# Optimization experiments

Measured on AMD Instinct MI355X. Metric: run time of the kernel, lower is better.

The kernel has to match this reference:

```python
import jax, jax.numpy as jnp
import numpy as np

C = 512
B, H, W = 4, 64, 64
GROUPS = 32
EPS = 1e-6
SCALE = 1.0 / np.sqrt(C)


def setup_inputs() -> dict:
    key = jax.random.key(0)
    ks = jax.random.split(key, 3)
    x = jax.random.normal(ks[0], (B, C, H, W), dtype=jnp.float32)
    # conv weights: kaiming-ish small init for numerical sanity
    qkv_w = jax.random.normal(ks[1], (3 * C, C), dtype=jnp.float32) * (1.0 / np.sqrt(C))
    proj_w = jax.random.normal(ks[2], (C, C), dtype=jnp.float32) * (1.0 / np.sqrt(C))
    return {
        "x": x,
        "norm_w": jnp.ones((C,), jnp.float32),
        "norm_b": jnp.zeros((C,), jnp.float32),
        "qkv_w": qkv_w,
        "qkv_b": jnp.zeros((3 * C,), jnp.float32),
        "proj_w": proj_w,
        "proj_b": jnp.zeros((C,), jnp.float32),
    }


def reference(x, norm_w, norm_b, qkv_w, qkv_b, proj_w, proj_b):
    b, c, h, w = x.shape
    hw = h * w
    # GroupNorm(32, eps=1e-6, affine)
    xg = x.reshape(b, GROUPS, -1)                       # [B, G, (C/G)*H*W]
    mean = jnp.mean(xg, axis=-1, keepdims=True)
    var = jnp.var(xg, axis=-1, keepdims=True)
    xn = ((xg - mean) * jax.lax.rsqrt(var + EPS)).reshape(b, c, h, w)
    xn = xn * norm_w[:, None, None] + norm_b[:, None, None]
    # 1x1 conv qkv == channel matmul
    qkv = jnp.einsum('oc,bchw->bohw', qkv_w, xn) + qkv_b[:, None, None]
    q, k, v = jnp.split(qkv, 3, axis=1)                 # each [B, C, H, W]
    q = q.reshape(b, c, hw)                              # [B, C, HW]
    k = k.reshape(b, c, hw)
    v = v.reshape(b, c, hw)
    # attn[b, i, j] = softmax_j( q_i . k_j * scale )
    scores = jnp.einsum('bci,bcj->bij', q, k) * SCALE    # [B, HW, HW]
    attn = jax.nn.softmax(scores, axis=-1)
    # h[b, c, i] = sum_j v[b, c, j] * attn[b, i, j]
    hmap = jnp.einsum('bcj,bij->bci', v, attn).reshape(b, c, h, w)
    out = x + jnp.einsum('oc,bchw->bohw', proj_w, hmap) + proj_b[:, None, None]
    return out
```

## Files before the change

kernel.cpp:

```cpp
#include <hip/hip_runtime.h>
#include <hip/hip_fp8.h>
#include <cstdint>
#include <cmath>

#define B_   4
#define C_   512
#define HW_  4096
#define G_   32
#define CPG_ 16
#define EPS_ 1e-6f
#define SCALE_ 0.04419417382415922f
#define PSCALE_ 0.0625f
#define SEXPC_ 0.063758715306f


typedef __bf16 bf16_t;
typedef __bf16 bf16x8 __attribute__((ext_vector_type(8)));
typedef float  f32x4  __attribute__((ext_vector_type(4)));
typedef int    i32x4  __attribute__((ext_vector_type(4)));
typedef int    i32x8  __attribute__((ext_vector_type(8)));
typedef unsigned int u32;
typedef __hip_fp8_e4m3 fp8_t;

__device__ __forceinline__ void cp16(const void* g, void* l) {
  __builtin_amdgcn_global_load_lds((__attribute__((address_space(1))) u32*)(g),
                                   (__attribute__((address_space(3))) u32*)(l),
                                   16, 0, 0);
}

__device__ __forceinline__ float fexp2(float x) {
  float r;
  asm("v_exp_f32 %0, %1\n\ts_nop 1" : "=v"(r) : "v"(x));
  return r;
}

__device__ __forceinline__ void zero_acc(f32x4 acc[4][4]) {
  f32x4 z = {0.f, 0.f, 0.f, 0.f};
#pragma unroll
  for (int i = 0; i < 4; ++i)
#pragma unroll
    for (int j = 0; j < 4; ++j) acc[i][j] = z;
}

template <bool ROWSUM, int SA = 0x7F, int SB = 0x7F>
__device__ __forceinline__ void gemm_bt_mx(const unsigned char* __restrict__ A,
                                           const unsigned char* __restrict__ B,
                                           int K, int lda, int ldb,
                                           f32x4 acc[4][4], f32x4 accl[4],
                                           unsigned char* AsB, unsigned char* BsB) {
  const int tid  = threadIdx.x;
  const int wave = tid >> 6;
  const int lane = tid & 63;
  const int wm = (wave >> 1) * 64;
  const int wn = (wave & 1) * 64;
  const int srow = lane >> 3;
  const int gch  = ((lane & 7) - srow) & 7;
  const unsigned char* gA = A + (size_t)(wave * 32 + srow) * lda + gch * 16;
  const unsigned char* gB = B + (size_t)(wave * 32 + srow) * ldb + gch * 16;
  const int lofs = wave * 32 * 128;
  const int fr = lane & 15;
  const int q  = lane >> 4;
  const int co0 = ((2 * q     + fr) & 7) * 16;
  const int co1 = ((2 * q + 1 + fr) & 7) * 16;
  const i32x8 vones = {0x38383838, 0x38383838, 0x38383838, 0x38383838,
                       0x38383838, 0x38383838, 0x38383838, 0x38383838};

  const int nT = K >> 7;
#pragma unroll
  for (int cc = 0; cc < 4; ++cc) {
    cp16(gA + (size_t)(cc * 8) * lda, AsB + lofs + cc * 1024);
    cp16(gB + (size_t)(cc * 8) * ldb, BsB + lofs + cc * 1024);
  }
  gA += 128; gB += 128;

#pragma unroll 1
  for (int t = 0; t < nT; ++t) {
    const int cur = t & 1;
    if (t + 1 < nT) {
#pragma unroll
      for (int cc = 0; cc < 4; ++cc) {
        cp16(gA + (size_t)(cc * 8) * lda, AsB + (cur ^ 1) * 16384 + lofs + cc * 1024);
        cp16(gB + (size_t)(cc * 8) * ldb, BsB + (cur ^ 1) * 16384 + lofs + cc * 1024);
      }
      gA += 128; gB += 128;
      asm volatile("s_waitcnt vmcnt(8)" ::: "memory");
    } else {
      asm volatile("s_waitcnt vmcnt(0)" ::: "memory");
    }
    __builtin_amdgcn_s_barrier();

    i32x8 a[4], b[4];
    const unsigned char* Ab = AsB + cur * 16384;
    const unsigned char* Bb = BsB + cur * 16384;
#pragma unroll
    for (int i = 0; i < 4; ++i) {
      const int ro = (wm + i * 16 + fr) * 128;
      i32x4 lo = *(const i32x4*)(Ab + ro + co0);
      i32x4 hi = *(const i32x4*)(Ab + ro + co1);
      a[i] = __builtin_shufflevector(lo, hi, 0, 1, 2, 3, 4, 5, 6, 7);
    }
#pragma unroll
    for (int j = 0; j < 4; ++j) {
      const int ro = (wn + j * 16 + fr) * 128;
      i32x4 lo = *(const i32x4*)(Bb + ro + co0);
      i32x4 hi = *(const i32x4*)(Bb + ro + co1);
      b[j] = __builtin_shufflevector(lo, hi, 0, 1, 2, 3, 4, 5, 6, 7);
    }
    __builtin_amdgcn_s_setprio(1);
#pragma unroll
    for (int i = 0; i < 4; ++i) {
#pragma unroll
      for (int j = 0; j < 4; ++j)
        acc[i][j] = __builtin_amdgcn_mfma_scale_f32_16x16x128_f8f6f4(
            a[i], b[j], acc[i][j], 0, 0, 0, SA, 0, SB);
      if (ROWSUM)
        accl[i] = __builtin_amdgcn_mfma_scale_f32_16x16x128_f8f6f4(
            a[i], vones, accl[i], 0, 0, 0, SA, 0, 0x7F);
    }
    __builtin_amdgcn_s_setprio(0);
    __builtin_amdgcn_s_barrier();
  }
}


__global__ void __launch_bounds__(256) prep_kernel(const float* __restrict__ x,
                                                   float* __restrict__ stats,
                                                   const float* __restrict__ qkv_w,
                                                   const float* __restrict__ proj_w,
                                                   fp8_t* __restrict__ wqkv8,
                                                   fp8_t* __restrict__ wproj8) {
  __shared__ float rs[256], rss[256];
  const int n = blockIdx.x;
  if (n < 1024) {
    const int bg = n >> 3;
    const int ch = n & 7;
    const float4* base = (const float4*)(x + (size_t)bg * (CPG_ * HW_)) +
                         (size_t)ch * (CPG_ * HW_ / 4 / 8);
    float s = 0.f, ss = 0.f;
    for (int i = threadIdx.x; i < CPG_ * HW_ / 4 / 8; i += 256) {
      float4 v = base[i];
      s  += v.x + v.y + v.z + v.w;
      ss += v.x * v.x + v.y * v.y + v.z * v.z + v.w * v.w;
    }
    rs[threadIdx.x] = s; rss[threadIdx.x] = ss;
    __syncthreads();
    for (int st = 128; st > 0; st >>= 1) {
      if ((int)threadIdx.x < st) {
        rs[threadIdx.x]  += rs[threadIdx.x + st];
        rss[threadIdx.x] += rss[threadIdx.x + st];
      }
      __syncthreads();
    }
    if (threadIdx.x == 0) {
      atomicAdd(&stats[bg * 2 + 0], rs[0]);
      atomicAdd(&stats[bg * 2 + 1], rss[0]);
    }
  } else {
    const int idx = (n - 1024) * 256 + threadIdx.x;
    const int t = idx * 4;
    const int nq = 1536 * 512;
    if (t < nq) {
      u32 dw = 0;
      dw = (u32)__builtin_amdgcn_cvt_pk_fp8_f32(qkv_w[t] * 16.f, qkv_w[t + 1] * 16.f, (int)dw, false);
      dw = (u32)__builtin_amdgcn_cvt_pk_fp8_f32(qkv_w[t + 2] * 16.f, qkv_w[t + 3] * 16.f, (int)dw, true);
      *(u32*)((unsigned char*)wqkv8 + t) = dw;
    } else {
      const int tt = t - nq;
      const int o = tt >> 9;
      const int p = tt & 511;
      float v[4];
#pragma unroll
      for (int e = 0; e < 4; ++e) {
        const int pe = p + e;
        const int off = pe & 63;
        const int c = (pe & ~63) + ((off & 3) << 4) + (off >> 2);
        v[e] = proj_w[(o << 9) + c] * 16.f;
      }
      u32 dw = 0;
      dw = (u32)__builtin_amdgcn_cvt_pk_fp8_f32(v[0], v[1], (int)dw, false);
      dw = (u32)__builtin_amdgcn_cvt_pk_fp8_f32(v[2], v[3], (int)dw, true);
      *(u32*)((unsigned char*)wproj8 + tt) = dw;
    }
  }
}

__global__ void __launch_bounds__(256) norm_tr_kernel(const float* __restrict__ x,
                                                      const float* __restrict__ stats,
                                                      const float* __restrict__ nw,
                                                      const float* __restrict__ nb,
                                                      fp8_t* __restrict__ xnT8) {
  __shared__ float tile[64][65];
  const int b  = blockIdx.z;
  const int i0 = blockIdx.x * 64;
  const int c0 = blockIdx.y * 64;
  const int tx = threadIdx.x & 63;
  const int ty = threadIdx.x >> 6;
  const int cbase = c0 + ty * 16;
  const int g = cbase >> 4;
  const float inv = 1.f / (float)(CPG_ * HW_);
  const float sum  = stats[(b * G_ + g) * 2 + 0];
  const float ssum = stats[(b * G_ + g) * 2 + 1];
  const float mean = sum * inv;
  const float rstd = rsqrtf(ssum * inv - mean * mean + EPS_);
#pragma unroll
  for (int r = 0; r < 16; ++r) {
    const int c = cbase + r;
    float v = x[((size_t)b * C_ + c) * HW_ + i0 + tx];
    tile[ty * 16 + r][tx] = (v - mean) * rstd * nw[c] + nb[c];
  }
  __syncthreads();
  const int il = threadIdx.x >> 2;
  const int q4 = threadIdx.x & 3;
#pragma unroll
  for (int m = 0; m < 4; ++m) {
    const int cq = q4 + m * 4;
    u32 dw = 0;
    dw = (u32)__builtin_amdgcn_cvt_pk_fp8_f32(tile[cq * 4 + 0][il], tile[cq * 4 + 1][il], (int)dw, false);
    dw = (u32)__builtin_amdgcn_cvt_pk_fp8_f32(tile[cq * 4 + 2][il], tile[cq * 4 + 3][il], (int)dw, true);
    *(u32*)((unsigned char*)xnT8 + ((size_t)b * HW_ + i0 + il) * C_ + c0 + cq * 4) = dw;
  }
}


__global__ void __launch_bounds__(256) qkv_gemm_kernel(const fp8_t* __restrict__ xnT8,
                                                       const fp8_t* __restrict__ wqkv8,
                                                       const float* __restrict__ qkv_b,
                                                       fp8_t* __restrict__ QKt8,
                                                       fp8_t* __restrict__ V8) {
  __shared__ __align__(16) unsigned char As[2 * 16384];
  __shared__ __align__(16) unsigned char Bs[2 * 16384];
  const int n = blockIdx.x;
  const int lane = threadIdx.x & 63, wave = threadIdx.x >> 6;
  const int wm = (wave >> 1) * 64, wn = (wave & 1) * 64;
  const int fr = lane & 15, q = lane >> 4;
  f32x4 acc[4][4]; zero_acc(acc);

  if (n < 1024) {
    const int xb = n & 7, yb = (n >> 3) & 31, b = n >> 8;
    const unsigned char* A  = (const unsigned char*)xnT8 + ((size_t)b * HW_ + yb * 128) * C_;
    const unsigned char* Bp = (const unsigned char*)wqkv8 + (size_t)xb * 128 * C_;
    gemm_bt_mx<false, 0x7F, 0x7B>(A, Bp, C_, C_, C_, acc, nullptr, As, Bs);
    const int r0 = yb * 128 + wm + (q << 2);
    const int cb = xb * 128 + wn;
    float bias[4];
#pragma unroll
    for (int j = 0; j < 4; ++j) bias[j] = qkv_b[cb + fr + j * 16];
#pragma unroll
    for (int i = 0; i < 4; ++i)
#pragma unroll
      for (int r = 0; r < 4; ++r) {
        const int row = r0 + i * 16 + r;
        u32 dw = 0;
        dw = (u32)__builtin_amdgcn_cvt_pk_fp8_f32(acc[i][0][r] + bias[0],
                                                  acc[i][1][r] + bias[1], (int)dw, false);
        dw = (u32)__builtin_amdgcn_cvt_pk_fp8_f32(acc[i][2][r] + bias[2],
                                                  acc[i][3][r] + bias[3], (int)dw, true);
        *(u32*)((unsigned char*)QKt8 + ((size_t)b * HW_ + row) * 1024 + cb + fr * 4) = dw;
      }
  } else {
    const int m = n - 1024;
    const int xb = m & 31, yb = (m >> 5) & 3, b = m >> 7;
    const unsigned char* A  = (const unsigned char*)wqkv8 + (size_t)(1024 + yb * 128) * C_;
    const unsigned char* Bp = (const unsigned char*)xnT8 + ((size_t)b * HW_ + xb * 128) * C_;
    gemm_bt_mx<false, 0x7B, 0x7F>(A, Bp, C_, C_, C_, acc, nullptr, As, Bs);
    const int r0 = yb * 128 + wm + (q << 2);
    const int cb = xb * 128 + wn;
#pragma unroll
    for (int i = 0; i < 4; ++i)
#pragma unroll
      for (int r = 0; r < 4; ++r) {
        const int row = r0 + i * 16 + r;
        const float bias = qkv_b[1024 + row];
        u32 dw = 0;
        dw = (u32)__builtin_amdgcn_cvt_pk_fp8_f32(acc[i][0][r] + bias,
                                                  acc[i][1][r] + bias, (int)dw, false);
        dw = (u32)__builtin_amdgcn_cvt_pk_fp8_f32(acc[i][2][r] + bias,
                                                  acc[i][3][r] + bias, (int)dw, true);
        *(u32*)((unsigned char*)V8 + ((size_t)b * C_ + row) * HW_ + cb + fr * 4) = dw;
      }
  }
}

__global__ void __launch_bounds__(256) sexp_gemm_kernel(const fp8_t* __restrict__ QKt8,
                                                        fp8_t* __restrict__ P8) {
  __shared__ __align__(16) unsigned char As[2 * 16384];
  __shared__ __align__(16) unsigned char Bs[2 * 16384];
  const int n   = blockIdx.x;
  const int xcd = n & 7;
  const int p   = n >> 3;
  const int xb  = p & 31;
  const int grp = xcd * 16 + (p >> 5);
  const int yb  = grp & 31;
  const int b   = grp >> 5;

  const unsigned char* QKtb = (const unsigned char*)QKt8 + (size_t)b * HW_ * 1024;
  fp8_t* Pb = P8 + (size_t)b * HW_ * HW_;
  f32x4 acc[4][4]; zero_acc(acc);
  const unsigned char* A  = QKtb + (size_t)yb * 128 * 1024;
  const unsigned char* Bp = QKtb + 512 + (size_t)xb * 128 * 1024;
  gemm_bt_mx<false>(A, Bp, 512, 1024, 1024, acc, nullptr, As, Bs);
  const int lane = threadIdx.x & 63, wave = threadIdx.x >> 6;
  const int wm = (wave >> 1) * 64, wn = (wave & 1) * 64;
  const int fr = lane & 15, q = lane >> 4;
  const int r0 = yb * 128 + wm + (q << 2);
  const int cb = xb * 128 + wn;
#pragma unroll
  for (int i = 0; i < 4; ++i)
#pragma unroll
    for (int r = 0; r < 4; ++r) {
      const int row = r0 + i * 16 + r;
      float e0 = fexp2(fmaf(acc[i][0][r], SEXPC_, -4.0f));
      float e1 = fexp2(fmaf(acc[i][1][r], SEXPC_, -4.0f));
      float e2 = fexp2(fmaf(acc[i][2][r], SEXPC_, -4.0f));
      float e3 = fexp2(fmaf(acc[i][3][r], SEXPC_, -4.0f));
      u32 dw = 0;
      dw = (u32)__builtin_amdgcn_cvt_pk_fp8_f32(e0, e1, (int)dw, false);
      dw = (u32)__builtin_amdgcn_cvt_pk_fp8_f32(e2, e3, (int)dw, true);
      *(u32*)((unsigned char*)Pb + (size_t)row * HW_ + cb + fr * 4) = dw;
    }
}

__global__ void __launch_bounds__(256) pv_gemm_kernel(const fp8_t* __restrict__ P8,
                                                      const fp8_t* __restrict__ V8,
                                                      fp8_t* __restrict__ hmT8) {
  __shared__ __align__(16) unsigned char As[2 * 16384];
  __shared__ __align__(16) unsigned char Bs[2 * 16384];
  const int n   = blockIdx.x;
  const int xcd = n & 7;
  const int p   = n >> 3;
  const int xb  = p & 3;
  const int grp = xcd * 16 + (p >> 2);
  const int yb  = grp & 31;
  const int b   = grp >> 5;

  const unsigned char* A  = (const unsigned char*)P8 + (size_t)b * HW_ * HW_ +
                            (size_t)yb * 128 * HW_;
  const unsigned char* Bp = (const unsigned char*)V8 + (size_t)b * C_ * HW_ +
                            (size_t)xb * 128 * HW_;
  fp8_t* hmTb = hmT8 + (size_t)b * HW_ * C_;

  f32x4 acc[4][4]; zero_acc(acc);
  f32x4 accl[4];
  {
    f32x4 z = {0.f, 0.f, 0.f, 0.f};
#pragma unroll
    for (int i = 0; i < 4; ++i) accl[i] = z;
  }
  gemm_bt_mx<true>(A, Bp, HW_, HW_, HW_, acc, accl, As, Bs);

  const int lane = threadIdx.x & 63, wave = threadIdx.x >> 6;
  const int wm = (wave >> 1) * 64, wn = (wave & 1) * 64;
  const int fr = lane & 15, q = lane >> 4;
  const int r0 = yb * 128 + wm + (q << 2);
  const int cb = xb * 128 + wn;
#pragma unroll
  for (int i = 0; i < 4; ++i)
#pragma unroll
    for (int r = 0; r < 4; ++r) {
      const int row = r0 + i * 16 + r;
      const float rl = 16.f * __builtin_amdgcn_rcpf(accl[i][r]);
      u32 dw = 0;
      dw = (u32)__builtin_amdgcn_cvt_pk_fp8_f32(acc[i][0][r] * rl, acc[i][1][r] * rl, (int)dw, false);
      dw = (u32)__builtin_amdgcn_cvt_pk_fp8_f32(acc[i][2][r] * rl, acc[i][3][r] * rl, (int)dw, true);
      *(u32*)((unsigned char*)hmTb + (size_t)row * C_ + cb + fr * 4) = dw;
    }
}

__global__ void __launch_bounds__(256) proj_gemm_kernel(const fp8_t* __restrict__ wproj8,
                                                        const fp8_t* __restrict__ hmT8,
                                                        const float* __restrict__ proj_b,
                                                        const float* __restrict__ x,
                                                        float* __restrict__ out) {
  __shared__ __align__(16) unsigned char As[2 * 16384];
  __shared__ __align__(16) unsigned char Bs[2 * 16384];
  const int b = blockIdx.z;
  f32x4 acc[4][4]; zero_acc(acc);
  const unsigned char* A  = (const unsigned char*)wproj8 + (size_t)blockIdx.y * 128 * C_;
  const unsigned char* Bp = (const unsigned char*)hmT8 + ((size_t)b * HW_ + blockIdx.x * 128) * C_;
  gemm_bt_mx<false, 0x7B, 0x7B>(A, Bp, C_, C_, C_, acc, nullptr, As, Bs);
  const int lane = threadIdx.x & 63, wave = threadIdx.x >> 6;
  const int wm = (wave >> 1) * 64, wn = (wave & 1) * 64;
  const int r0 = blockIdx.y * 128 + wm + ((lane >> 4) << 2);
  const int c0 = blockIdx.x * 128 + wn + (lane & 15);
#pragma unroll
  for (int i = 0; i < 4; ++i)
#pragma unroll
    for (int r = 0; r < 4; ++r) {
      const int row = r0 + i * 16 + r;
      const float bias = proj_b[row];
#pragma unroll
      for (int j = 0; j < 4; ++j) {
        const int col = c0 + j * 16;
        const size_t idx = ((size_t)b * C_ + row) * HW_ + col;
        out[idx] = x[idx] + bias + acc[i][j][r];
      }
    }
}

extern "C" void kernel_launch(void* const* d_in, const int* in_sizes, int n_in,
                              void* d_out, int out_size, void* d_ws, size_t ws_size,
                              hipStream_t stream) {
  const float* x      = (const float*)d_in[0];
  const float* norm_w = (const float*)d_in[1];
  const float* norm_b = (const float*)d_in[2];
  const float* qkv_w  = (const float*)d_in[3];
  const float* qkv_b  = (const float*)d_in[4];
  const float* proj_w = (const float*)d_in[5];
  const float* proj_b = (const float*)d_in[6];
  float* out = (float*)d_out;

  char* ws = (char*)d_ws;
  size_t o = 0;
  fp8_t* wqkv8  = (fp8_t*)(ws + o); o += (size_t)1536 * 512;
  fp8_t* wproj8 = (fp8_t*)(ws + o); o += (size_t)512 * 512;
  float* stats  = (float*)(ws + o); o += 128 * 2 * 4;
  fp8_t* xnT8   = (fp8_t*)(ws + o); o += (size_t)B_ * HW_ * C_;
  fp8_t* QKt8   = (fp8_t*)(ws + o); o += (size_t)B_ * HW_ * 1024;
  fp8_t* V8     = (fp8_t*)(ws + o); o += (size_t)B_ * C_ * HW_;
  fp8_t* hmT8   = (fp8_t*)(ws + o); o += (size_t)B_ * HW_ * C_;
  fp8_t* P8     = (fp8_t*)(ws + o); o += (size_t)B_ * HW_ * HW_;

  hipMemsetAsync(stats, 0, 128 * 2 * sizeof(float), stream);
  prep_kernel<<<2048, 256, 0, stream>>>(x, stats, qkv_w, proj_w, wqkv8, wproj8);
  norm_tr_kernel<<<dim3(HW_ / 64, C_ / 64, B_), 256, 0, stream>>>(x, stats, norm_w, norm_b, xnT8);
  qkv_gemm_kernel<<<1536, 256, 0, stream>>>(xnT8, wqkv8, qkv_b, QKt8, V8);
  sexp_gemm_kernel<<<4096, 256, 0, stream>>>(QKt8, P8);
  pv_gemm_kernel<<<512, 256, 0, stream>>>(P8, V8, hmT8);
  proj_gemm_kernel<<<dim3(HW_ / 128, C_ / 128, B_), 256, 0, stream>>>(
      wproj8, hmT8, proj_b, x, out);
}
```

Before: 229.7 us.

## Enlarge score GEMM tiles to 256x256 with 512-thread blocks and custom pipelined loop

The QK^T/softmax-exp GEMM moves from 128x128 tiles with 256 threads to 256x256 tiles with 512 threads (8 waves, 128x64 per wave). It gets a hand-written double-buffered K loop with XOR-swizzled LDS staging, prefetch interleaved with MFMA phases, and setprio around the MFMAs. The goal is to halve global/LDS traffic per output and cut block count, at the cost of 128KB LDS per block and higher register pressure from 32 accumulators.

```diff
diff --git a/kernel.cpp b/kernel.cpp
--- a/kernel.cpp
+++ b/kernel.cpp
@@ -281,31 +281,111 @@
   }
 }
 
-__global__ void __launch_bounds__(256) sexp_gemm_kernel(const fp8_t* __restrict__ QKt8,
-                                                        fp8_t* __restrict__ P8) {
-  __shared__ __align__(16) unsigned char As[2 * 16384];
-  __shared__ __align__(16) unsigned char Bs[2 * 16384];
+__global__ void __launch_bounds__(512, 2) sexp_gemm_kernel(const fp8_t* __restrict__ QKt8,
+                                                           fp8_t* __restrict__ P8) {
+  __shared__ __align__(16) unsigned char As[2][256 * 128];
+  __shared__ __align__(16) unsigned char Bs[2][256 * 128];
+
   const int n   = blockIdx.x;
   const int xcd = n & 7;
   const int p   = n >> 3;
-  const int xb  = p & 31;
-  const int grp = xcd * 16 + (p >> 5);
-  const int yb  = grp & 31;
-  const int b   = grp >> 5;
+  const int xb  = p & 15;
+  const int grp = xcd * 8 + (p >> 4);
+  const int yb  = grp & 15;
+  const int b   = grp >> 4;
 
   const unsigned char* QKtb = (const unsigned char*)QKt8 + (size_t)b * HW_ * 1024;
+  const unsigned char* Agl = QKtb + (size_t)yb * 256 * 1024;
+  const unsigned char* Bgl = QKtb + 512 + (size_t)xb * 256 * 1024;
+
+  const int tid  = threadIdx.x;
+  const int lane = tid & 63;
+  const int wave = tid >> 6;
+  const int wm   = (wave >> 2) * 128;
+  const int wn   = (wave & 3) * 64;
+  const int fr   = lane & 15;
+  const int q    = lane >> 4;
+  const int co0  = ((2 * q     + fr) & 7) * 16;
+  const int co1  = ((2 * q + 1 + fr) & 7) * 16;
+
+  const int srow = tid >> 3;
+  const int sch  = tid & 7;
+  const int gch  = (((sch - srow) & 7)) * 16;
+
+  f32x4 acc[8][4];
+  {
+    f32x4 z = {0.f, 0.f, 0.f, 0.f};
+#pragma unroll
+    for (int i = 0; i < 8; ++i)
+#pragma unroll
+      for (int j = 0; j < 4; ++j) acc[i][j] = z;
+  }
+
+#pragma unroll
+  for (int s = 0; s < 4; ++s) {
+    const int row = s * 64 + srow;
+    cp16(Agl + (size_t)row * 1024 + gch, &As[0][row * 128 + sch * 16]);
+    cp16(Bgl + (size_t)row * 1024 + gch, &Bs[0][row * 128 + sch * 16]);
+  }
+  asm volatile("s_waitcnt vmcnt(0)" ::: "memory");
+  __builtin_amdgcn_s_barrier();
+
+#pragma unroll 1
+  for (int t = 0; t < 4; ++t) {
+    const int cur = t & 1;
+    const unsigned char* Ab = As[cur];
+    const unsigned char* Bb = Bs[cur];
+#pragma unroll
+    for (int ph = 0; ph < 4; ++ph) {
+      const int ah = (ph & 1) * 4;
+      const int bh = (ph >> 1) * 2;
+      i32x8 a[4], bfr[2];
+#pragma unroll
+      for (int i = 0; i < 4; ++i) {
+        const int ro = (wm + (ah + i) * 16 + fr) * 128;
+        i32x4 lo = *(const i32x4*)(Ab + ro + co0);
+        i32x4 hi = *(const i32x4*)(Ab + ro + co1);
+        a[i] = __builtin_shufflevector(lo, hi, 0, 1, 2, 3, 4, 5, 6, 7);
+      }
+#pragma unroll
+      for (int j = 0; j < 2; ++j) {
+        const int ro = (wn + (bh + j) * 16 + fr) * 128;
+        i32x4 lo = *(const i32x4*)(Bb + ro + co0);
+        i32x4 hi = *(const i32x4*)(Bb + ro + co1);
+        bfr[j] = __builtin_shufflevector(lo, hi, 0, 1, 2, 3, 4, 5, 6, 7);
+      }
+      if (t < 3 && ph < 2) {
+#pragma unroll
+        for (int s = 0; s < 2; ++s) {
+          const int row = (ph * 2 + s) * 64 + srow;
+          cp16(Agl + (size_t)row * 1024 + (t + 1) * 128 + gch,
+               &As[cur ^ 1][row * 128 + sch * 16]);
+          cp16(Bgl + (size_t)row * 1024 + (t + 1) * 128 + gch,
+               &Bs[cur ^ 1][row * 128 + sch * 16]);
+        }
+      }
+      __builtin_amdgcn_s_barrier();
+      asm volatile("s_waitcnt lgkmcnt(0)" ::: "memory");
+      __builtin_amdgcn_sched_barrier(0);
+      __builtin_amdgcn_s_setprio(1);
+#pragma unroll
+      for (int i = 0; i < 4; ++i)
+#pragma unroll
+        for (int j = 0; j < 2; ++j)
+          acc[ah + i][bh + j] = __builtin_amdgcn_mfma_scale_f32_16x16x128_f8f6f4(
+              a[i], bfr[j], acc[ah + i][bh + j], 0, 0, 0, 0x7F, 0, 0x7F);
+      __builtin_amdgcn_s_setprio(0);
+      if (ph == 3)
+        asm volatile("s_waitcnt vmcnt(0)" ::: "memory");
+      __builtin_amdgcn_s_barrier();
+    }
+  }
+
   fp8_t* Pb = P8 + (size_t)b * HW_ * HW_;
-  f32x4 acc[4][4]; zero_acc(acc);
-  const unsigned char* A  = QKtb + (size_t)yb * 128 * 1024;
-  const unsigned char* Bp = QKtb + 512 + (size_t)xb * 128 * 1024;
-  gemm_bt_mx<false>(A, Bp, 512, 1024, 1024, acc, nullptr, As, Bs);
-  const int lane = threadIdx.x & 63, wave = threadIdx.x >> 6;
-  const int wm = (wave >> 1) * 64, wn = (wave & 1) * 64;
-  const int fr = lane & 15, q = lane >> 4;
-  const int r0 = yb * 128 + wm + (q << 2);
-  const int cb = xb * 128 + wn;
-#pragma unroll
-  for (int i = 0; i < 4; ++i)
+  const int r0 = yb * 256 + wm + (q << 2);
+  const int cb = xb * 256 + wn;
+#pragma unroll
+  for (int i = 0; i < 8; ++i)
 #pragma unroll
     for (int r = 0; r < 4; ++r) {
       const int row = r0 + i * 16 + r;
@@ -424,7 +504,7 @@
   prep_kernel<<<2048, 256, 0, stream>>>(x, stats, qkv_w, proj_w, wqkv8, wproj8);
   norm_tr_kernel<<<dim3(HW_ / 64, C_ / 64, B_), 256, 0, stream>>>(x, stats, norm_w, norm_b, xnT8);
   qkv_gemm_kernel<<<1536, 256, 0, stream>>>(xnT8, wqkv8, qkv_b, QKt8, V8);
-  sexp_gemm_kernel<<<4096, 256, 0, stream>>>(QKt8, P8);
+  sexp_gemm_kernel<<<1024, 512, 0, stream>>>(QKt8, P8);
   pv_gemm_kernel<<<512, 256, 0, stream>>>(P8, V8, hmT8);
   proj_gemm_kernel<<<dim3(HW_ / 128, C_ / 128, B_), 256, 0, stream>>>(
       wproj8, hmT8, proj_b, x, out);
```

Measured after the change: 237.6 us. +3.4%, slower.

## Software-pipeline LDS fragment reads with register double-buffering in FP8 GEMM loop

Applied to the files above, without the earlier changes.

Restructures the shared FP8 GEMM main loop so that the next tile's LDS fragments are read into a second register set while the current tile's MFMAs run. The global-to-LDS prefetch moves two tiles ahead, with a single barrier per step. The loop is unrolled by two with ping-pong register and LDS buffers. Launch bounds also gain a minimum of 2 blocks per SM on all GEMM kernels. This doubles the fragment registers and may add register pressure or spills, and the unroll-by-2 assumes an even tile count.

```diff
diff --git a/kernel.cpp b/kernel.cpp
--- a/kernel.cpp
+++ b/kernel.cpp
@@ -41,6 +41,50 @@
 #pragma unroll
     for (int j = 0; j < 4; ++j) acc[i][j] = z;
 }
+
+
+#define GEMM_STEP(tt, ac, bc, an, bn, rdA, rdB, stA, stB)                      \
+  {                                                                            \
+    asm volatile("s_waitcnt vmcnt(0)" ::: "memory");                           \
+    __builtin_amdgcn_s_barrier();                                              \
+    if ((tt) + 2 < nT) {                                                       \
+      _Pragma("unroll")                                                        \
+      for (int cc = 0; cc < 4; ++cc) {                                         \
+        cp16(gA + (size_t)(cc * 8) * lda, (stA) + lofs + cc * 1024);           \
+        cp16(gB + (size_t)(cc * 8) * ldb, (stB) + lofs + cc * 1024);           \
+      }                                                                        \
+      gA += 128; gB += 128;                                                    \
+    }                                                                          \
+    if ((tt) + 1 < nT) {                                                       \
+      _Pragma("unroll")                                                        \
+      for (int i = 0; i < 4; ++i) {                                            \
+        const int ro = (wm + i * 16 + fr) * 128;                               \
+        i32x4 lo = *(const i32x4*)((rdA) + ro + co0);                          \
+        i32x4 hi = *(const i32x4*)((rdA) + ro + co1);                          \
+        an[i] = __builtin_shufflevector(lo, hi, 0, 1, 2, 3, 4, 5, 6, 7);       \
+      }                                                                        \
+      _Pragma("unroll")                                                        \
+      for (int j = 0; j < 4; ++j) {                                            \
+        const int ro = (wn + j * 16 + fr) * 128;                               \
+        i32x4 lo = *(const i32x4*)((rdB) + ro + co0);                          \
+        i32x4 hi = *(const i32x4*)((rdB) + ro + co1);                          \
+        bn[j] = __builtin_shufflevector(lo, hi, 0, 1, 2, 3, 4, 5, 6, 7);       \
+      }                                                                        \
+    }                                                                          \
+    __builtin_amdgcn_s_setprio(1);                                             \
+    _Pragma("unroll")                                                          \
+    for (int i = 0; i < 4; ++i) {                                              \
+      _Pragma("unroll")                                                        \
+      for (int j = 0; j < 4; ++j)                                              \
+        acc[i][j] = __builtin_amdgcn_mfma_scale_f32_16x16x128_f8f6f4(          \
+            ac[i], bc[j], acc[i][j], 0, 0, 0, SA, 0, SB);                      \
+      if (ROWSUM)                                                              \
+        accl[i] = __builtin_amdgcn_mfma_scale_f32_16x16x128_f8f6f4(            \
+            ac[i], vones, accl[i], 0, 0, 0, SA, 0, 0x7F);                      \
+    }                                                                          \
+    __builtin_amdgcn_s_setprio(0);                                             \
+    asm volatile("s_waitcnt lgkmcnt(0)" ::: "memory");                         \
+  }
 
 template <bool ROWSUM, int SA = 0x7F, int SB = 0x7F>
 __device__ __forceinline__ void gemm_bt_mx(const unsigned char* __restrict__ A,
@@ -72,53 +116,36 @@
     cp16(gB + (size_t)(cc * 8) * ldb, BsB + lofs + cc * 1024);
   }
   gA += 128; gB += 128;
+#pragma unroll
+  for (int cc = 0; cc < 4; ++cc) {
+    cp16(gA + (size_t)(cc * 8) * lda, AsB + 16384 + lofs + cc * 1024);
+    cp16(gB + (size_t)(cc * 8) * ldb, BsB + 16384 + lofs + cc * 1024);
+  }
+  gA += 128; gB += 128;
+  asm volatile("s_waitcnt vmcnt(8)" ::: "memory");
+  __builtin_amdgcn_s_barrier();
+
+  i32x8 a0[4], b0[4], a1[4], b1[4];
+#pragma unroll
+  for (int i = 0; i < 4; ++i) {
+    const int ro = (wm + i * 16 + fr) * 128;
+    i32x4 lo = *(const i32x4*)(AsB + ro + co0);
+    i32x4 hi = *(const i32x4*)(AsB + ro + co1);
+    a0[i] = __builtin_shufflevector(lo, hi, 0, 1, 2, 3, 4, 5, 6, 7);
+  }
+#pragma unroll
+  for (int j = 0; j < 4; ++j) {
+    const int ro = (wn + j * 16 + fr) * 128;
+    i32x4 lo = *(const i32x4*)(BsB + ro + co0);
+    i32x4 hi = *(const i32x4*)(BsB + ro + co1);
+    b0[j] = __builtin_shufflevector(lo, hi, 0, 1, 2, 3, 4, 5, 6, 7);
+  }
+  asm volatile("s_waitcnt lgkmcnt(0)" ::: "memory");
 
 #pragma unroll 1
-  for (int t = 0; t < nT; ++t) {
-    const int cur = t & 1;
-    if (t + 1 < nT) {
-#pragma unroll
-      for (int cc = 0; cc < 4; ++cc) {
-        cp16(gA + (size_t)(cc * 8) * lda, AsB + (cur ^ 1) * 16384 + lofs + cc * 1024);
-        cp16(gB + (size_t)(cc * 8) * ldb, BsB + (cur ^ 1) * 16384 + lofs + cc * 1024);
-      }
-      gA += 128; gB += 128;
-      asm volatile("s_waitcnt vmcnt(8)" ::: "memory");
-    } else {
-      asm volatile("s_waitcnt vmcnt(0)" ::: "memory");
-    }
-    __builtin_amdgcn_s_barrier();
-
-    i32x8 a[4], b[4];
-    const unsigned char* Ab = AsB + cur * 16384;
-    const unsigned char* Bb = BsB + cur * 16384;
-#pragma unroll
-    for (int i = 0; i < 4; ++i) {
-      const int ro = (wm + i * 16 + fr) * 128;
-      i32x4 lo = *(const i32x4*)(Ab + ro + co0);
-      i32x4 hi = *(const i32x4*)(Ab + ro + co1);
-      a[i] = __builtin_shufflevector(lo, hi, 0, 1, 2, 3, 4, 5, 6, 7);
-    }
-#pragma unroll
-    for (int j = 0; j < 4; ++j) {
-      const int ro = (wn + j * 16 + fr) * 128;
-      i32x4 lo = *(const i32x4*)(Bb + ro + co0);
-      i32x4 hi = *(const i32x4*)(Bb + ro + co1);
-      b[j] = __builtin_shufflevector(lo, hi, 0, 1, 2, 3, 4, 5, 6, 7);
-    }
-    __builtin_amdgcn_s_setprio(1);
-#pragma unroll
-    for (int i = 0; i < 4; ++i) {
-#pragma unroll
-      for (int j = 0; j < 4; ++j)
-        acc[i][j] = __builtin_amdgcn_mfma_scale_f32_16x16x128_f8f6f4(
-            a[i], b[j], acc[i][j], 0, 0, 0, SA, 0, SB);
-      if (ROWSUM)
-        accl[i] = __builtin_amdgcn_mfma_scale_f32_16x16x128_f8f6f4(
-            a[i], vones, accl[i], 0, 0, 0, SA, 0, 0x7F);
-    }
-    __builtin_amdgcn_s_setprio(0);
-    __builtin_amdgcn_s_barrier();
+  for (int t = 0; t < nT; t += 2) {
+    GEMM_STEP(t,     a0, b0, a1, b1, AsB + 16384, BsB + 16384, AsB,         BsB);
+    GEMM_STEP(t + 1, a1, b1, a0, b0, AsB,         BsB,         AsB + 16384, BsB + 16384);
   }
 }
 
@@ -222,11 +249,11 @@
 }
 
 
-__global__ void __launch_bounds__(256) qkv_gemm_kernel(const fp8_t* __restrict__ xnT8,
-                                                       const fp8_t* __restrict__ wqkv8,
-                                                       const float* __restrict__ qkv_b,
-                                                       fp8_t* __restrict__ QKt8,
-                                                       fp8_t* __restrict__ V8) {
+__global__ void __launch_bounds__(256, 2) qkv_gemm_kernel(const fp8_t* __restrict__ xnT8,
+                                                          const fp8_t* __restrict__ wqkv8,
+                                                          const float* __restrict__ qkv_b,
+                                                          fp8_t* __restrict__ QKt8,
+                                                          fp8_t* __restrict__ V8) {
   __shared__ __align__(16) unsigned char As[2 * 16384];
   __shared__ __align__(16) unsigned char Bs[2 * 16384];
   const int n = blockIdx.x;
@@ -281,8 +308,8 @@
   }
 }
 
-__global__ void __launch_bounds__(256) sexp_gemm_kernel(const fp8_t* __restrict__ QKt8,
-                                                        fp8_t* __restrict__ P8) {
+__global__ void __launch_bounds__(256, 2) sexp_gemm_kernel(const fp8_t* __restrict__ QKt8,
+                                                           fp8_t* __restrict__ P8) {
   __shared__ __align__(16) unsigned char As[2 * 16384];
   __shared__ __align__(16) unsigned char Bs[2 * 16384];
   const int n   = blockIdx.x;
@@ -320,9 +347,9 @@
     }
 }
 
-__global__ void __launch_bounds__(256) pv_gemm_kernel(const fp8_t* __restrict__ P8,
-                                                      const fp8_t* __restrict__ V8,
-                                                      fp8_t* __restrict__ hmT8) {
+__global__ void __launch_bounds__(256, 2) pv_gemm_kernel(const fp8_t* __restrict__ P8,
+                                                         const fp8_t* __restrict__ V8,
+                                                         fp8_t* __restrict__ hmT8) {
   __shared__ __align__(16) unsigned char As[2 * 16384];
   __shared__ __align__(16) unsigned char Bs[2 * 16384];
   const int n   = blockIdx.x;
@@ -366,11 +393,11 @@
     }
 }
 
-__global__ void __launch_bounds__(256) proj_gemm_kernel(const fp8_t* __restrict__ wproj8,
-                                                        const fp8_t* __restrict__ hmT8,
-                                                        const float* __restrict__ proj_b,
-                                                        const float* __restrict__ x,
-                                                        float* __restrict__ out) {
+__global__ void __launch_bounds__(256, 2) proj_gemm_kernel(const fp8_t* __restrict__ wproj8,
+                                                           const fp8_t* __restrict__ hmT8,
+                                                           const float* __restrict__ proj_b,
+                                                           const float* __restrict__ x,
+                                                           float* __restrict__ out) {
   __shared__ __align__(16) unsigned char As[2 * 16384];
   __shared__ __align__(16) unsigned char Bs[2 * 16384];
   const int b = blockIdx.z;
```

Result: slower. 338.3 us (+47.3%).
